# Kernel optimization log

Hardware: AMD Instinct MI355X
Metric: run time of the kernel (lower is better)

## Reference

```python
import jax, jax.numpy as jnp
import numpy as np

B, S, H = 1, 2048, 4096
NH = 32
HD = H // NH  # 128
HALF = HD // 2
BASE = 10000.0


def setup_inputs() -> dict:
    key = jax.random.key(0)
    k1, k2, k3 = jax.random.split(key, 3)
    hidden_states = jax.random.normal(k1, (B, S, H), dtype=jnp.float32)
    W_qkv = jax.random.normal(k2, (H, 3 * H), dtype=jnp.float32) * 0.02
    W_o = jax.random.normal(k3, (H, H), dtype=jnp.float32) * 0.02
    # causal additive mask [B,1,S,S]: 0 on/below diagonal, large negative above
    causal = jnp.triu(jnp.full((S, S), -1e9, dtype=jnp.float32), k=1)
    attention_mask = jnp.broadcast_to(causal[None, None], (B, 1, S, S))
    position_ids = jnp.broadcast_to(jnp.arange(S, dtype=jnp.int64)[None, :], (B, S))
    return {
        'hidden_states': hidden_states,
        'W_qkv': W_qkv,
        'W_o': W_o,
        'attention_mask': attention_mask,
        'position_ids': position_ids,
    }


def _rope(x, cos, sin):
    # x: [b,s,nh,hd]; cos/sin: [b,s,1,half]. Half-split rotation as in the Triton kernel.
    x1, x2 = x[..., :HALF], x[..., HALF:]
    return jnp.concatenate([x1 * cos - x2 * sin, x1 * sin + x2 * cos], axis=-1)


def reference(hidden_states, W_qkv, W_o, attention_mask, position_ids):
    b, s, h = hidden_states.shape
    # fused QKV projection (dequantized GPTQ matmul == dense matmul math)
    qkv = jnp.einsum('bsh,hk->bsk', hidden_states, W_qkv).reshape(b, s, 3, NH, HD)
    # RoPE angles: freq = exp(col * INV_BASE) * position_id, INV_BASE = -2 ln(base)/head_dim
    inv_base = -2.0 * np.log(BASE) / HD
    freqs = jnp.exp(jnp.arange(HALF, dtype=jnp.float32) * inv_base)  # [half]
    theta = position_ids.astype(jnp.float32)[:, :, None] * freqs      # [b,s,half]
    cos = jnp.cos(theta)[:, :, None, :]
    sin = jnp.sin(theta)[:, :, None, :]
    q = _rope(qkv[:, :, 0], cos, sin).transpose(0, 2, 1, 3)  # [b,nh,s,hd]
    k = _rope(qkv[:, :, 1], cos, sin).transpose(0, 2, 1, 3)
    v = qkv[:, :, 2].transpose(0, 2, 1, 3)
    scores = jnp.einsum('bhqd,bhkd->bhqk', q, k) / np.sqrt(HD).astype(np.float32)
    scores = scores + attention_mask
    scores = jnp.maximum(scores, jnp.finfo(scores.dtype).min)
    attn = jax.nn.softmax(scores.astype(jnp.float32), axis=-1).astype(q.dtype)
    out = jnp.einsum('bhqk,bhkd->bqhd', attn, v).reshape(b, s, h)
    return jnp.einsum('bsh,ho->bso', out, W_o)
```

## Files before the change

### kernel.cpp

```cpp
#include <hip/hip_runtime.h>

#define S_LEN 2048
#define HDIM 4096
#define NHEADS 32
#define HEAD_DIM 128
#define HALF_DIM 64
#define N_QKV 12288
#define QK_COLS 8192

typedef __attribute__((ext_vector_type(8))) short short8;
typedef __attribute__((ext_vector_type(4))) float f32x4;

typedef const __attribute__((address_space(1))) unsigned int gu32;
typedef __attribute__((address_space(3))) unsigned int lu32;

__device__ __forceinline__ void gload_lds16(const void* g, void* l) {
    __builtin_amdgcn_global_load_lds((gu32*)g, (lu32*)l, 16, 0, 0);
}

__device__ __forceinline__ unsigned short f2bf(float f) {
    unsigned int u = __float_as_uint(f);
    u += 0x7fff + ((u >> 16) & 1);
    return (unsigned short)(u >> 16);
}

__device__ __forceinline__ void xcd_map(int& bx, int& by) {
    int gx = gridDim.x;
    int lin = blockIdx.y * gx + blockIdx.x;
    int x = lin & 7, c = lin >> 3;
    int bxp = gx >> 3;
    bx = bxp * x + c % bxp;
    by = c / bxp;
}


__global__ __launch_bounds__(256) void cvt_hs_k(const float* __restrict__ in,
                                                unsigned short* __restrict__ out, int n4) {
    int i = blockIdx.x * 256 + threadIdx.x;
    if (i >= n4) return;
    float4 v = reinterpret_cast<const float4*>(in)[i];
    ushort4 o;
    o.x = f2bf(v.x); o.y = f2bf(v.y); o.z = f2bf(v.z); o.w = f2bf(v.w);
    reinterpret_cast<ushort4*>(out)[i] = o;
}

__device__ __forceinline__ int permute_col(int n) {
    if (n < QK_COLS) {
        int hd = n & 127;
        int base = n - hd;
        int e = hd & 63;
        int d2 = (e & 15) + 32 * (e >> 4) + ((hd >> 6) << 4);
        return base + d2;
    }
    return n;
}

template <bool PERM>
__global__ __launch_bounds__(256) void tconv_k(const float* __restrict__ in,
                                               unsigned short* __restrict__ out, int R, int C) {
    __shared__ float tile[64][65];
    int c0 = blockIdx.x * 64, r0 = blockIdx.y * 64;
    int tx = threadIdx.x & 63, ty = threadIdx.x >> 6;
#pragma unroll
    for (int i = 0; i < 16; ++i) {
        int r = ty + i * 4;
        tile[r][tx] = in[(size_t)(r0 + r) * C + c0 + tx];
    }
    __syncthreads();
#pragma unroll
    for (int i = 0; i < 16; ++i) {
        int c = ty + i * 4;
        int n = PERM ? permute_col(c0 + c) : (c0 + c);
        out[(size_t)n * R + r0 + tx] = f2bf(tile[tx][c]);
    }
}

__global__ __launch_bounds__(256) void rope_tab_k(const int* __restrict__ pos_raw,
                                                  float* __restrict__ ctab,
                                                  float* __restrict__ stab) {
    int i = blockIdx.x * 256 + threadIdx.x;
    int s = i >> 6, d = i & 63;
    bool is64 = (pos_raw[1] == 0 && pos_raw[2] == 1);
    int p = is64 ? pos_raw[2 * s] : pos_raw[s];
    const float INVB = -0.14391156831212787f;
    float freq = expf((float)d * INVB);
    float th = (float)p * freq;
    ctab[i] = cosf(th);
    stab[i] = sinf(th);
}


__device__ __forceinline__ void mainloop(const unsigned short* __restrict__ Ag,
                                         const unsigned short* __restrict__ Bg,
                                         int K, int m0, int n0,
                                         char* As, char* Bs,
                                         f32x4 (&acc)[4][4]) {
    const int tid = threadIdx.x;
    const int wid = tid >> 6, lane = tid & 63, l15 = lane & 15, l4 = lane >> 4;
    const int wm = wid >> 1, wn = wid & 1;
    const int NT = K >> 6;

    size_t abase[4], bbase[4];
    int off[4];
#pragma unroll
    for (int i = 0; i < 4; ++i) {
        int p = (i * 256 + tid) << 4;
        int q = p ^ (((p >> 7) & 7) << 4);
        abase[i] = (size_t)(m0 + (q >> 7)) * K + ((q & 127) >> 1);
        bbase[i] = (size_t)(n0 + (q >> 7)) * K + ((q & 127) >> 1);
        off[i] = p;
    }

    for (int t = 0; t < NT; ++t) {
        int k0 = t << 6;
#pragma unroll
        for (int i = 0; i < 4; ++i) gload_lds16(Ag + abase[i] + k0, As + off[i]);
#pragma unroll
        for (int i = 0; i < 4; ++i) gload_lds16(Bg + bbase[i] + k0, Bs + off[i]);
        asm volatile("s_waitcnt vmcnt(0)" ::: "memory");
        __builtin_amdgcn_s_barrier();

        short8 a[4][2], b[4][2];
#pragma unroll
        for (int am = 0; am < 4; ++am)
#pragma unroll
            for (int ks = 0; ks < 2; ++ks) {
                int lin = ((wm * 64 + am * 16 + l15) << 7) + ks * 64 + l4 * 16;
                a[am][ks] = *(const short8*)(As + (lin ^ (((lin >> 7) & 7) << 4)));
            }
#pragma unroll
        for (int bn = 0; bn < 4; ++bn)
#pragma unroll
            for (int ks = 0; ks < 2; ++ks) {
                int lin = ((wn * 64 + bn * 16 + l15) << 7) + ks * 64 + l4 * 16;
                b[bn][ks] = *(const short8*)(Bs + (lin ^ (((lin >> 7) & 7) << 4)));
            }
#pragma unroll
        for (int ks = 0; ks < 2; ++ks)
#pragma unroll
            for (int am = 0; am < 4; ++am)
#pragma unroll
                for (int bn = 0; bn < 4; ++bn)
                    acc[am][bn] = __builtin_amdgcn_mfma_f32_16x16x32_bf16(a[am][ks], b[bn][ks], acc[am][bn], 0, 0, 0);

        __builtin_amdgcn_s_barrier();
    }
}

__global__ __launch_bounds__(256, 3) void gemm1_k(const unsigned short* __restrict__ A,
                                                  const unsigned short* __restrict__ Bt,
                                                  const float* __restrict__ ctab,
                                                  const float* __restrict__ stab,
                                                  unsigned short* __restrict__ qb,
                                                  unsigned short* __restrict__ kb,
                                                  unsigned short* __restrict__ vt) {
    __shared__ __attribute__((aligned(16))) char As[16384];
    __shared__ __attribute__((aligned(16))) char Bs[16384];

    int bx, by;
    xcd_map(bx, by);
    int m0 = by * 128, n0 = bx * 128;

    f32x4 acc[4][4];
#pragma unroll
    for (int i = 0; i < 4; ++i)
#pragma unroll
        for (int j = 0; j < 4; ++j) acc[i][j] = (f32x4){0.f, 0.f, 0.f, 0.f};

    mainloop(A, Bt, HDIM, m0, n0, As, Bs, acc);

    int tid = threadIdx.x, wid = tid >> 6, lane = tid & 63, l15 = lane & 15, l4 = lane >> 4;
    int wm = wid >> 1, wn = wid & 1;
    int which = n0 >> 12;
    int head = (n0 & 4095) >> 7;
    if (which < 2) {
        unsigned short* dst = which ? kb : qb;
#pragma unroll
        for (int am = 0; am < 4; ++am)
#pragma unroll
            for (int j = 0; j < 4; ++j) {
                int s = m0 + wm * 64 + am * 16 + l4 * 4 + j;
#pragma unroll
                for (int p = 0; p < 2; ++p) {
                    float x1 = acc[am][2 * p][j], x2 = acc[am][2 * p + 1][j];
                    int e = l15 + 16 * (2 * wn + p);
                    float cs = ctab[s * 64 + e], sn = stab[s * 64 + e];
                    dst[((size_t)head * S_LEN + s) * HEAD_DIM + e] = f2bf(x1 * cs - x2 * sn);
                    dst[((size_t)head * S_LEN + s) * HEAD_DIM + e + 64] = f2bf(x1 * sn + x2 * cs);
                }
            }
    } else {
#pragma unroll
        for (int am = 0; am < 4; ++am)
#pragma unroll
            for (int j = 0; j < 4; ++j) {
                int s = m0 + wm * 64 + am * 16 + l4 * 4 + j;
#pragma unroll
                for (int bn = 0; bn < 4; ++bn) {
                    int d = wn * 64 + bn * 16 + l15;
                    vt[((size_t)head * HEAD_DIM + d) * S_LEN + s] = f2bf(acc[am][bn][j]);
                }
            }
    }
}

__global__ __launch_bounds__(256, 3) void gemm2_k(const unsigned short* __restrict__ A,
                                                  const unsigned short* __restrict__ Bt,
                                                  float* __restrict__ out) {
    __shared__ __attribute__((aligned(16))) char As[16384];
    __shared__ __attribute__((aligned(16))) char Bs[16384];

    int bx, by;
    xcd_map(bx, by);
    int m0 = by * 128, n0 = bx * 128;

    f32x4 acc[4][4];
#pragma unroll
    for (int i = 0; i < 4; ++i)
#pragma unroll
        for (int j = 0; j < 4; ++j) acc[i][j] = (f32x4){0.f, 0.f, 0.f, 0.f};

    mainloop(A, Bt, HDIM, m0, n0, As, Bs, acc);

    int tid = threadIdx.x, wid = tid >> 6, lane = tid & 63, l15 = lane & 15, l4 = lane >> 4;
    int wm = wid >> 1, wn = wid & 1;
#pragma unroll
    for (int am = 0; am < 4; ++am)
#pragma unroll
        for (int j = 0; j < 4; ++j) {
            int s = m0 + wm * 64 + am * 16 + l4 * 4 + j;
#pragma unroll
            for (int bn = 0; bn < 4; ++bn)
                out[(size_t)s * HDIM + n0 + wn * 64 + bn * 16 + l15] = acc[am][bn][j];
        }
}

__global__ __launch_bounds__(256) void flash_k(const unsigned short* __restrict__ Q,
                                               const unsigned short* __restrict__ Kb,
                                               const unsigned short* __restrict__ Vt,
                                               float* __restrict__ O_parts,
                                               float* __restrict__ ml) {
    __shared__ __attribute__((aligned(16))) char Ks[2][16384];
    __shared__ __attribute__((aligned(16))) char Vs[2][16384];
    __shared__ __attribute__((aligned(16))) char Ps[4][4096];
    int h = blockIdx.y;
    int bx2 = 39 - (int)blockIdx.x;
    int qblk, spl;
    if (bx2 < 4)       { qblk = bx2;                 spl = 0; }
    else if (bx2 < 12) { qblk = 4 + ((bx2 - 4) >> 1);  spl = (bx2 - 4) & 1; }
    else if (bx2 < 24) { int u = bx2 - 12; int q3 = u / 3; qblk = 8 + q3; spl = u - 3 * q3; }
    else               { qblk = 12 + ((bx2 - 24) >> 2); spl = (bx2 - 24) & 3; }
    int pidx = h * 40 + bx2;
    int kv_start = spl << 9;
    int kv_end = min((qblk + 1) << 7, (spl + 1) << 9);
    int NT = (kv_end - kv_start) >> 6;

    int tid = threadIdx.x, w = tid >> 6, lane = tid & 63, l15 = lane & 15, l4 = lane >> 4;
    int qrow0 = qblk * 128 + w * 32;

    const unsigned short* Kg = Kb + (size_t)h * S_LEN * HEAD_DIM;
    const unsigned short* Vg = Vt + (size_t)h * HEAD_DIM * S_LEN;

    short8 qf[2][4];
#pragma unroll
    for (int mt = 0; mt < 2; ++mt) {
        int s = qrow0 + mt * 16 + l15;
#pragma unroll
        for (int ks = 0; ks < 4; ++ks)
            qf[mt][ks] = *(const short8*)(Q + ((size_t)h * S_LEN + s) * HEAD_DIM + ks * 32 + l4 * 8);
    }

    float m_run[2][4];
    f32x4 o[2][8];
    f32x4 lsum[2];
#pragma unroll
    for (int mt = 0; mt < 2; ++mt) {
#pragma unroll
        for (int j = 0; j < 4; ++j) m_run[mt][j] = -1e30f;
        lsum[mt] = (f32x4){0.f, 0.f, 0.f, 0.f};
#pragma unroll
        for (int dt = 0; dt < 8; ++dt) o[mt][dt] = (f32x4){0.f, 0.f, 0.f, 0.f};
    }

    int lofs[4];
    size_t kgofs[4], vgofs[4];
#pragma unroll
    for (int i = 0; i < 4; ++i) {
        int p = (i * 256 + tid) << 4;
        lofs[i] = p;
        int qk = p ^ (((p >> 8) & 7) << 4);
        kgofs[i] = (size_t)(qk >> 8) * HEAD_DIM + ((qk & 255) >> 1);
        int qv = p ^ (((p >> 7) & 7) << 4);
        vgofs[i] = (size_t)(qv >> 7) * S_LEN + ((qv & 127) >> 1);
    }

    auto stage = [&](int t) {
        char* Kd = Ks[t & 1];
        char* Vd = Vs[t & 1];
        size_t kvoff = (size_t)(kv_start + t * 64);
#pragma unroll
        for (int i = 0; i < 4; ++i) gload_lds16(Kg + kvoff * HEAD_DIM + kgofs[i], Kd + lofs[i]);
#pragma unroll
        for (int i = 0; i < 4; ++i) gload_lds16(Vg + kvoff + vgofs[i], Vd + lofs[i]);
    };

    const float scale = 0.08838834764831845f;

    short8 onesv;
#pragma unroll
    for (int e = 0; e < 8; ++e) onesv[e] = (short)0x3F80;

    stage(0);

    for (int t = 0; t < NT; ++t) {
        int cur = t & 1;
        asm volatile("s_waitcnt vmcnt(0)" ::: "memory");
        __builtin_amdgcn_s_barrier();
        __builtin_amdgcn_sched_barrier(0);
        if (t + 1 < NT) stage(t + 1);

        f32x4 sc[2][4];
#pragma unroll
        for (int mt = 0; mt < 2; ++mt)
#pragma unroll
            for (int nt = 0; nt < 4; ++nt) sc[mt][nt] = (f32x4){0.f, 0.f, 0.f, 0.f};
#pragma unroll
        for (int ks = 0; ks < 4; ++ks) {
            short8 kfr[4];
#pragma unroll
            for (int nt = 0; nt < 4; ++nt) {
                int lin = ((nt * 16 + l15) << 8) + ks * 64 + l4 * 16;
                kfr[nt] = *(const short8*)(Ks[cur] + (lin ^ (((lin >> 8) & 7) << 4)));
            }
#pragma unroll
            for (int mt = 0; mt < 2; ++mt)
#pragma unroll
                for (int nt = 0; nt < 4; ++nt)
                    sc[mt][nt] = __builtin_amdgcn_mfma_f32_16x16x32_bf16(qf[mt][ks], kfr[nt], sc[mt][nt], 0, 0, 0);
        }

        float pmax[2][4];
        bool need = false;
#pragma unroll
        for (int mt = 0; mt < 2; ++mt)
#pragma unroll
            for (int j = 0; j < 4; ++j) {
                int srow = qrow0 + mt * 16 + l4 * 4 + j;
                int c = kv_start + t * 64 + l15;
                float v0 = (c      <= srow) ? sc[mt][0][j] * scale : -1e30f;
                float v1 = (c + 16 <= srow) ? sc[mt][1][j] * scale : -1e30f;
                float v2 = (c + 32 <= srow) ? sc[mt][2][j] * scale : -1e30f;
                float v3 = (c + 48 <= srow) ? sc[mt][3][j] * scale : -1e30f;
                sc[mt][0][j] = v0; sc[mt][1][j] = v1; sc[mt][2][j] = v2; sc[mt][3][j] = v3;
                float mx = fmaxf(fmaxf(v0, v1), fmaxf(v2, v3));
                mx = fmaxf(mx, __shfl_xor(mx, 1));
                mx = fmaxf(mx, __shfl_xor(mx, 2));
                mx = fmaxf(mx, __shfl_xor(mx, 4));
                mx = fmaxf(mx, __shfl_xor(mx, 8));
                pmax[mt][j] = mx;
                need = need || (mx > m_run[mt][j] + 8.0f);
            }
        if (__any(need ? 1 : 0)) {
#pragma unroll
            for (int mt = 0; mt < 2; ++mt)
#pragma unroll
                for (int j = 0; j < 4; ++j) {
                    float mnew = fmaxf(m_run[mt][j], pmax[mt][j]);
                    float r = __expf(m_run[mt][j] - mnew);
                    m_run[mt][j] = mnew;
                    lsum[mt][j] *= r;
#pragma unroll
                    for (int dt = 0; dt < 8; ++dt) o[mt][dt][j] *= r;
                }
        }

#pragma unroll
        for (int mt = 0; mt < 2; ++mt)
#pragma unroll
            for (int j = 0; j < 4; ++j) {
                int prow = mt * 16 + l4 * 4 + j;
                int rb = prow << 7;
                int sw = (prow & 7) << 4;
#pragma unroll
                for (int nt = 0; nt < 4; ++nt) {
                    unsigned short pb = f2bf(__expf(sc[mt][nt][j] - m_run[mt][j]));
                    *(unsigned short*)(Ps[w] + ((rb + (l15 + nt * 16) * 2) ^ sw)) = pb;
                }
            }
        asm volatile("s_waitcnt lgkmcnt(0)" ::: "memory");
        __builtin_amdgcn_sched_barrier(0);

        short8 pf[2][2];
#pragma unroll
        for (int mt = 0; mt < 2; ++mt)
#pragma unroll
            for (int k2 = 0; k2 < 2; ++k2) {
                int lin = ((mt * 16 + l15) << 7) + k2 * 64 + l4 * 16;
                pf[mt][k2] = *(const short8*)(Ps[w] + (lin ^ (((lin >> 7) & 7) << 4)));
            }
#pragma unroll
        for (int k2 = 0; k2 < 2; ++k2)
#pragma unroll
            for (int mt = 0; mt < 2; ++mt)
                lsum[mt] = __builtin_amdgcn_mfma_f32_16x16x32_bf16(pf[mt][k2], onesv, lsum[mt], 0, 0, 0);
#pragma unroll
        for (int dt = 0; dt < 8; ++dt) {
#pragma unroll
            for (int k2 = 0; k2 < 2; ++k2) {
                int lin = ((dt * 16 + l15) << 7) + k2 * 64 + l4 * 16;
                short8 vf = *(const short8*)(Vs[cur] + (lin ^ (((lin >> 7) & 7) << 4)));
#pragma unroll
                for (int mt = 0; mt < 2; ++mt)
                    o[mt][dt] = __builtin_amdgcn_mfma_f32_16x16x32_bf16(pf[mt][k2], vf, o[mt][dt], 0, 0, 0);
            }
        }
    }

    float* Op = O_parts + (size_t)pidx * 16384;
#pragma unroll
    for (int mt = 0; mt < 2; ++mt)
#pragma unroll
        for (int j = 0; j < 4; ++j) {
            int rloc = w * 32 + mt * 16 + l4 * 4 + j;
#pragma unroll
            for (int dt = 0; dt < 8; ++dt)
                Op[rloc * 128 + dt * 16 + l15] = o[mt][dt][j];
            if (l15 == 0) {
                ml[(size_t)pidx * 256 + rloc] = m_run[mt][j];
                ml[(size_t)pidx * 256 + 128 + rloc] = lsum[mt][j];
            }
        }
}

__global__ __launch_bounds__(256) void reduce_k(const float* __restrict__ Op,
                                                const float* __restrict__ ml,
                                                unsigned short* __restrict__ ctx) {
    int qblk = blockIdx.x, h = blockIdx.y;
    int ns = (qblk >> 2) + 1;
    int st;
    if (qblk < 4) st = qblk;
    else if (qblk < 8) st = 4 + 2 * (qblk - 4);
    else if (qblk < 12) st = 12 + 3 * (qblk - 8);
    else st = 24 + 4 * (qblk - 12);
    int p0 = h * 40 + st;
#pragma unroll
    for (int it = 0; it < 16; ++it) {
        int idx = it * 256 + threadIdx.x;
        int row = idx >> 5, dq = idx & 31;
        float mstar = -1e30f;
        for (int s = 0; s < ns; ++s)
            mstar = fmaxf(mstar, ml[(size_t)(p0 + s) * 256 + row]);
        f32x4 acc = (f32x4){0.f, 0.f, 0.f, 0.f};
        float lt = 0.f;
        for (int s = 0; s < ns; ++s) {
            float wgt = __expf(ml[(size_t)(p0 + s) * 256 + row] - mstar);
            lt += wgt * ml[(size_t)(p0 + s) * 256 + 128 + row];
            f32x4 ov = *(const f32x4*)(Op + (size_t)(p0 + s) * 16384 + row * 128 + dq * 4);
            acc += ov * wgt;
        }
        float inv = 1.0f / lt;
        int grow = qblk * 128 + row;
        ushort4 o4;
        o4.x = f2bf(acc[0] * inv);
        o4.y = f2bf(acc[1] * inv);
        o4.z = f2bf(acc[2] * inv);
        o4.w = f2bf(acc[3] * inv);
        *(ushort4*)(ctx + (size_t)grow * HDIM + h * 128 + dq * 4) = o4;
    }
}


extern "C" void kernel_launch(void* const* d_in, const int* in_sizes, int n_in,
                              void* d_out, int out_size, void* d_ws, size_t ws_size,
                              hipStream_t stream) {
    const float* hs = (const float*)d_in[0];
    const float* wqkv = (const float*)d_in[1];
    const float* wo = (const float*)d_in[2];
    const int* pos = (const int*)d_in[4];
    float* out = (float*)d_out;
    char* ws = (char*)d_ws;
    const size_t MB = 1024 * 1024;

    unsigned short* hs_b = (unsigned short*)(ws);
    unsigned short* wq_t = (unsigned short*)(ws + 16 * MB);
    unsigned short* wo_t = (unsigned short*)(ws + 112 * MB);
    unsigned short* qbuf = (unsigned short*)(ws + 144 * MB);
    unsigned short* kbuf = (unsigned short*)(ws + 160 * MB);
    unsigned short* vtb  = (unsigned short*)(ws + 176 * MB);
    unsigned short* ctx  = (unsigned short*)(ws + 192 * MB);
    float* ctab = (float*)(ws + 208 * MB);
    float* stab = (float*)(ws + 209 * MB);
    float* O_parts = (float*)(ws + 16 * MB);
    float* ml_buf  = (float*)(ws + 96 * MB);

    cvt_hs_k<<<(S_LEN * HDIM / 4 + 255) / 256, 256, 0, stream>>>(hs, hs_b, S_LEN * HDIM / 4);
    tconv_k<true><<<dim3(N_QKV / 64, HDIM / 64), 256, 0, stream>>>(wqkv, wq_t, HDIM, N_QKV);
    tconv_k<false><<<dim3(HDIM / 64, HDIM / 64), 256, 0, stream>>>(wo, wo_t, HDIM, HDIM);
    rope_tab_k<<<(S_LEN * 64) / 256, 256, 0, stream>>>(pos, ctab, stab);
    gemm1_k<<<dim3(N_QKV / 128, S_LEN / 128), 256, 0, stream>>>(hs_b, wq_t, ctab, stab, qbuf, kbuf, vtb);
    flash_k<<<dim3(40, NHEADS), 256, 0, stream>>>(qbuf, kbuf, vtb, O_parts, ml_buf);
    reduce_k<<<dim3(S_LEN / 128, NHEADS), 256, 0, stream>>>(O_parts, ml_buf, ctx);
    gemm2_k<<<dim3(HDIM / 128, S_LEN / 128), 256, 0, stream>>>(ctx, wo_t, out);
}
```

Before: 541.7 us.

## Read K/V directly from global in flash kernel, drop LDS staging, remap grid

Removes the double-buffered LDS staging of K and V tiles in the flash attention kernel, so MFMA operands are loaded straight from global memory (relying on L2/cache reuse across the four waves). This drops the per-tile barrier and wait and cuts LDS use to allow two blocks per CU (launch_bounds 256,2). The grid becomes 1D, with the 8 heads that share a block index interleaved so blocks working on the same KV region run close together in time. The risk is more global/L1 traffic and higher load latency without LDS reuse across waves.

```diff
diff --git a/kernel.cpp b/kernel.cpp
--- a/kernel.cpp
+++ b/kernel.cpp
@@ -235,16 +235,16 @@
         }
 }
 
-__global__ __launch_bounds__(256) void flash_k(const unsigned short* __restrict__ Q,
-                                               const unsigned short* __restrict__ Kb,
-                                               const unsigned short* __restrict__ Vt,
-                                               float* __restrict__ O_parts,
-                                               float* __restrict__ ml) {
-    __shared__ __attribute__((aligned(16))) char Ks[2][16384];
-    __shared__ __attribute__((aligned(16))) char Vs[2][16384];
+__global__ __launch_bounds__(256, 2) void flash_k(const unsigned short* __restrict__ Q,
+                                                  const unsigned short* __restrict__ Kb,
+                                                  const unsigned short* __restrict__ Vt,
+                                                  float* __restrict__ O_parts,
+                                                  float* __restrict__ ml) {
     __shared__ __attribute__((aligned(16))) char Ps[4][4096];
-    int h = blockIdx.y;
-    int bx2 = 39 - (int)blockIdx.x;
+    int lin = blockIdx.x;
+    int c = lin >> 3;
+    int h = (lin & 7) + 8 * (c / 40);
+    int bx2 = 39 - (c % 40);
     int qblk, spl;
     if (bx2 < 4)       { qblk = bx2;                 spl = 0; }
     else if (bx2 < 12) { qblk = 4 + ((bx2 - 4) >> 1);  spl = (bx2 - 4) & 1; }
@@ -282,42 +282,15 @@
         for (int dt = 0; dt < 8; ++dt) o[mt][dt] = (f32x4){0.f, 0.f, 0.f, 0.f};
     }
 
-    int lofs[4];
-    size_t kgofs[4], vgofs[4];
-#pragma unroll
-    for (int i = 0; i < 4; ++i) {
-        int p = (i * 256 + tid) << 4;
-        lofs[i] = p;
-        int qk = p ^ (((p >> 8) & 7) << 4);
-        kgofs[i] = (size_t)(qk >> 8) * HEAD_DIM + ((qk & 255) >> 1);
-        int qv = p ^ (((p >> 7) & 7) << 4);
-        vgofs[i] = (size_t)(qv >> 7) * S_LEN + ((qv & 127) >> 1);
-    }
-
-    auto stage = [&](int t) {
-        char* Kd = Ks[t & 1];
-        char* Vd = Vs[t & 1];
-        size_t kvoff = (size_t)(kv_start + t * 64);
-#pragma unroll
-        for (int i = 0; i < 4; ++i) gload_lds16(Kg + kvoff * HEAD_DIM + kgofs[i], Kd + lofs[i]);
-#pragma unroll
-        for (int i = 0; i < 4; ++i) gload_lds16(Vg + kvoff + vgofs[i], Vd + lofs[i]);
-    };
-
     const float scale = 0.08838834764831845f;
 
     short8 onesv;
 #pragma unroll
     for (int e = 0; e < 8; ++e) onesv[e] = (short)0x3F80;
 
-    stage(0);
-
     for (int t = 0; t < NT; ++t) {
-        int cur = t & 1;
-        asm volatile("s_waitcnt vmcnt(0)" ::: "memory");
-        __builtin_amdgcn_s_barrier();
-        __builtin_amdgcn_sched_barrier(0);
-        if (t + 1 < NT) stage(t + 1);
+        int kv0 = kv_start + t * 64;
+        const unsigned short* Kt = Kg + (size_t)kv0 * HEAD_DIM;
 
         f32x4 sc[2][4];
 #pragma unroll
@@ -328,10 +301,8 @@
         for (int ks = 0; ks < 4; ++ks) {
             short8 kfr[4];
 #pragma unroll
-            for (int nt = 0; nt < 4; ++nt) {
-                int lin = ((nt * 16 + l15) << 8) + ks * 64 + l4 * 16;
-                kfr[nt] = *(const short8*)(Ks[cur] + (lin ^ (((lin >> 8) & 7) << 4)));
-            }
+            for (int nt = 0; nt < 4; ++nt)
+                kfr[nt] = *(const short8*)(Kt + (nt * 16 + l15) * HEAD_DIM + ks * 32 + l4 * 8);
 #pragma unroll
             for (int mt = 0; mt < 2; ++mt)
 #pragma unroll
@@ -346,11 +317,11 @@
 #pragma unroll
             for (int j = 0; j < 4; ++j) {
                 int srow = qrow0 + mt * 16 + l4 * 4 + j;
-                int c = kv_start + t * 64 + l15;
-                float v0 = (c      <= srow) ? sc[mt][0][j] * scale : -1e30f;
-                float v1 = (c + 16 <= srow) ? sc[mt][1][j] * scale : -1e30f;
-                float v2 = (c + 32 <= srow) ? sc[mt][2][j] * scale : -1e30f;
-                float v3 = (c + 48 <= srow) ? sc[mt][3][j] * scale : -1e30f;
+                int cc = kv0 + l15;
+                float v0 = (cc      <= srow) ? sc[mt][0][j] * scale : -1e30f;
+                float v1 = (cc + 16 <= srow) ? sc[mt][1][j] * scale : -1e30f;
+                float v2 = (cc + 32 <= srow) ? sc[mt][2][j] * scale : -1e30f;
+                float v3 = (cc + 48 <= srow) ? sc[mt][3][j] * scale : -1e30f;
                 sc[mt][0][j] = v0; sc[mt][1][j] = v1; sc[mt][2][j] = v2; sc[mt][3][j] = v3;
                 float mx = fmaxf(fmaxf(v0, v1), fmaxf(v2, v3));
                 mx = fmaxf(mx, __shfl_xor(mx, 1));
@@ -395,8 +366,8 @@
         for (int mt = 0; mt < 2; ++mt)
 #pragma unroll
             for (int k2 = 0; k2 < 2; ++k2) {
-                int lin = ((mt * 16 + l15) << 7) + k2 * 64 + l4 * 16;
-                pf[mt][k2] = *(const short8*)(Ps[w] + (lin ^ (((lin >> 7) & 7) << 4)));
+                int plin = ((mt * 16 + l15) << 7) + k2 * 64 + l4 * 16;
+                pf[mt][k2] = *(const short8*)(Ps[w] + (plin ^ (((plin >> 7) & 7) << 4)));
             }
 #pragma unroll
         for (int k2 = 0; k2 < 2; ++k2)
@@ -407,8 +378,7 @@
         for (int dt = 0; dt < 8; ++dt) {
 #pragma unroll
             for (int k2 = 0; k2 < 2; ++k2) {
-                int lin = ((dt * 16 + l15) << 7) + k2 * 64 + l4 * 16;
-                short8 vf = *(const short8*)(Vs[cur] + (lin ^ (((lin >> 7) & 7) << 4)));
+                short8 vf = *(const short8*)(Vg + (size_t)(dt * 16 + l15) * S_LEN + kv0 + k2 * 32 + l4 * 8);
 #pragma unroll
                 for (int mt = 0; mt < 2; ++mt)
                     o[mt][dt] = __builtin_amdgcn_mfma_f32_16x16x32_bf16(pf[mt][k2], vf, o[mt][dt], 0, 0, 0);
@@ -498,7 +468,7 @@
     tconv_k<false><<<dim3(HDIM / 64, HDIM / 64), 256, 0, stream>>>(wo, wo_t, HDIM, HDIM);
     rope_tab_k<<<(S_LEN * 64) / 256, 256, 0, stream>>>(pos, ctab, stab);
     gemm1_k<<<dim3(N_QKV / 128, S_LEN / 128), 256, 0, stream>>>(hs_b, wq_t, ctab, stab, qbuf, kbuf, vtb);
-    flash_k<<<dim3(40, NHEADS), 256, 0, stream>>>(qbuf, kbuf, vtb, O_parts, ml_buf);
+    flash_k<<<dim3(1280), 256, 0, stream>>>(qbuf, kbuf, vtb, O_parts, ml_buf);
     reduce_k<<<dim3(S_LEN / 128, NHEADS), 256, 0, stream>>>(O_parts, ml_buf, ctx);
     gemm2_k<<<dim3(HDIM / 128, S_LEN / 128), 256, 0, stream>>>(ctx, wo_t, out);
 }
```

Result: slower. 559.3 us (+3.3%).

## Single-buffer flash attention K/V tiles to raise occupancy to three blocks per CU

Applied to the files above, without the earlier changes.

Drops double buffering of the K/V LDS tiles, shrinking shared memory from about 80KB to 48KB per block, and adds a launch bound asking for three blocks per CU. Each iteration now loads its tile synchronously, waits, computes, then barriers before the next overwrite. Global offsets become 32-bit ints with the kv_start base folded into the pointers, which lowers register pressure. The intent is to hide memory latency through more resident blocks rather than an in-block prefetch, at the cost of losing load/compute overlap within each block and adding a second barrier per tile.

```diff
diff --git a/kernel.cpp b/kernel.cpp
--- a/kernel.cpp
+++ b/kernel.cpp
@@ -235,13 +235,13 @@
         }
 }
 
-__global__ __launch_bounds__(256) void flash_k(const unsigned short* __restrict__ Q,
-                                               const unsigned short* __restrict__ Kb,
-                                               const unsigned short* __restrict__ Vt,
-                                               float* __restrict__ O_parts,
-                                               float* __restrict__ ml) {
-    __shared__ __attribute__((aligned(16))) char Ks[2][16384];
-    __shared__ __attribute__((aligned(16))) char Vs[2][16384];
+__global__ __launch_bounds__(256, 3) void flash_k(const unsigned short* __restrict__ Q,
+                                                  const unsigned short* __restrict__ Kb,
+                                                  const unsigned short* __restrict__ Vt,
+                                                  float* __restrict__ O_parts,
+                                                  float* __restrict__ ml) {
+    __shared__ __attribute__((aligned(16))) char Ks[16384];
+    __shared__ __attribute__((aligned(16))) char Vs[16384];
     __shared__ __attribute__((aligned(16))) char Ps[4][4096];
     int h = blockIdx.y;
     int bx2 = 39 - (int)blockIdx.x;
@@ -258,8 +258,8 @@
     int tid = threadIdx.x, w = tid >> 6, lane = tid & 63, l15 = lane & 15, l4 = lane >> 4;
     int qrow0 = qblk * 128 + w * 32;
 
-    const unsigned short* Kg = Kb + (size_t)h * S_LEN * HEAD_DIM;
-    const unsigned short* Vg = Vt + (size_t)h * HEAD_DIM * S_LEN;
+    const unsigned short* Kg = Kb + (size_t)h * S_LEN * HEAD_DIM + (size_t)kv_start * HEAD_DIM;
+    const unsigned short* Vg = Vt + (size_t)h * HEAD_DIM * S_LEN + kv_start;
 
     short8 qf[2][4];
 #pragma unroll
@@ -282,27 +282,16 @@
         for (int dt = 0; dt < 8; ++dt) o[mt][dt] = (f32x4){0.f, 0.f, 0.f, 0.f};
     }
 
-    int lofs[4];
-    size_t kgofs[4], vgofs[4];
+    int lofs[4], kgofs[4], vgofs[4];
 #pragma unroll
     for (int i = 0; i < 4; ++i) {
         int p = (i * 256 + tid) << 4;
         lofs[i] = p;
         int qk = p ^ (((p >> 8) & 7) << 4);
-        kgofs[i] = (size_t)(qk >> 8) * HEAD_DIM + ((qk & 255) >> 1);
+        kgofs[i] = (qk >> 8) * HEAD_DIM + ((qk & 255) >> 1);
         int qv = p ^ (((p >> 7) & 7) << 4);
-        vgofs[i] = (size_t)(qv >> 7) * S_LEN + ((qv & 127) >> 1);
-    }
-
-    auto stage = [&](int t) {
-        char* Kd = Ks[t & 1];
-        char* Vd = Vs[t & 1];
-        size_t kvoff = (size_t)(kv_start + t * 64);
-#pragma unroll
-        for (int i = 0; i < 4; ++i) gload_lds16(Kg + kvoff * HEAD_DIM + kgofs[i], Kd + lofs[i]);
-#pragma unroll
-        for (int i = 0; i < 4; ++i) gload_lds16(Vg + kvoff + vgofs[i], Vd + lofs[i]);
-    };
+        vgofs[i] = (qv >> 7) * S_LEN + ((qv & 127) >> 1);
+    }
 
     const float scale = 0.08838834764831845f;
 
@@ -310,14 +299,14 @@
 #pragma unroll
     for (int e = 0; e < 8; ++e) onesv[e] = (short)0x3F80;
 
-    stage(0);
-
     for (int t = 0; t < NT; ++t) {
-        int cur = t & 1;
+        int kvt = t * 64;
+#pragma unroll
+        for (int i = 0; i < 4; ++i) gload_lds16(Kg + (size_t)kvt * HEAD_DIM + kgofs[i], Ks + lofs[i]);
+#pragma unroll
+        for (int i = 0; i < 4; ++i) gload_lds16(Vg + kvt + vgofs[i], Vs + lofs[i]);
         asm volatile("s_waitcnt vmcnt(0)" ::: "memory");
         __builtin_amdgcn_s_barrier();
-        __builtin_amdgcn_sched_barrier(0);
-        if (t + 1 < NT) stage(t + 1);
 
         f32x4 sc[2][4];
 #pragma unroll
@@ -330,7 +319,7 @@
 #pragma unroll
             for (int nt = 0; nt < 4; ++nt) {
                 int lin = ((nt * 16 + l15) << 8) + ks * 64 + l4 * 16;
-                kfr[nt] = *(const short8*)(Ks[cur] + (lin ^ (((lin >> 8) & 7) << 4)));
+                kfr[nt] = *(const short8*)(Ks + (lin ^ (((lin >> 8) & 7) << 4)));
             }
 #pragma unroll
             for (int mt = 0; mt < 2; ++mt)
@@ -346,11 +335,11 @@
 #pragma unroll
             for (int j = 0; j < 4; ++j) {
                 int srow = qrow0 + mt * 16 + l4 * 4 + j;
-                int c = kv_start + t * 64 + l15;
-                float v0 = (c      <= srow) ? sc[mt][0][j] * scale : -1e30f;
-                float v1 = (c + 16 <= srow) ? sc[mt][1][j] * scale : -1e30f;
-                float v2 = (c + 32 <= srow) ? sc[mt][2][j] * scale : -1e30f;
-                float v3 = (c + 48 <= srow) ? sc[mt][3][j] * scale : -1e30f;
+                int cc = kv_start + kvt + l15;
+                float v0 = (cc      <= srow) ? sc[mt][0][j] * scale : -1e30f;
+                float v1 = (cc + 16 <= srow) ? sc[mt][1][j] * scale : -1e30f;
+                float v2 = (cc + 32 <= srow) ? sc[mt][2][j] * scale : -1e30f;
+                float v3 = (cc + 48 <= srow) ? sc[mt][3][j] * scale : -1e30f;
                 sc[mt][0][j] = v0; sc[mt][1][j] = v1; sc[mt][2][j] = v2; sc[mt][3][j] = v3;
                 float mx = fmaxf(fmaxf(v0, v1), fmaxf(v2, v3));
                 mx = fmaxf(mx, __shfl_xor(mx, 1));
@@ -408,12 +397,13 @@
 #pragma unroll
             for (int k2 = 0; k2 < 2; ++k2) {
                 int lin = ((dt * 16 + l15) << 7) + k2 * 64 + l4 * 16;
-                short8 vf = *(const short8*)(Vs[cur] + (lin ^ (((lin >> 7) & 7) << 4)));
+                short8 vf = *(const short8*)(Vs + (lin ^ (((lin >> 7) & 7) << 4)));
 #pragma unroll
                 for (int mt = 0; mt < 2; ++mt)
                     o[mt][dt] = __builtin_amdgcn_mfma_f32_16x16x32_bf16(pf[mt][k2], vf, o[mt][dt], 0, 0, 0);
             }
         }
+        __builtin_amdgcn_s_barrier();
     }
 
     float* Op = O_parts + (size_t)pidx * 16384;
```

Result: slower. 792.9 us (+46.4%).
